# Performance work log

Measured on AMD Instinct MI355X. Metric: run time of the kernel, lower is better.

The kernel has to match this reference:

```python
import jax, jax.numpy as jnp
import numpy as np

B, C_IN, V, C_OUT, K = 4, 64, 50000, 128, 7


def setup_inputs() -> dict:
    key = jax.random.key(0)
    k1, k2, k3, k4 = jax.random.split(key, 4)
    x = jax.random.normal(k1, (B, C_IN, V, 1), dtype=jnp.float32)
    # Gi: per-vertex [self, n1, n2, n3] indices (random neighbors, in-range)
    Gi = jax.random.randint(k2, (B, V, 4), 0, V, dtype=jnp.int64)
    # Conv2d(in, out, kernel=(1,7)) weight collapsed to [out, in, 7]
    W = jax.random.normal(k3, (C_OUT, C_IN, K), dtype=jnp.float32) * 0.05
    b = jax.random.normal(k4, (C_OUT,), dtype=jnp.float32) * 0.05
    return {"x": x, "Gi": Gi, "W": W, "b": b}


def reference(x, Gi, W, b):
    xs = x[..., 0]  # [B, C, V]  (squeeze(-1))
    Bx, C, Vx = xs.shape
    # prepend zero-padding column (index 0 after Gi+1 maps padded -1 entries)
    xp = jnp.concatenate([jnp.zeros((Bx, C, 1), xs.dtype), xs], axis=2)  # [B,C,V+1]
    gi = Gi + 1
    # gather per batch: f[b,c,v,j] = xp[b,c,gi[b,v,j]]
    f = jax.vmap(lambda xb, gb: xb[:, gb])(xp, gi)  # [B, C, V, 4]
    f0, f1, f2, f3 = f[..., 0], f[..., 1], f[..., 2], f[..., 3]
    G = jnp.stack([
        f0,
        f1 + f2 + f3,                                        # symm_oper 1
        f1 * f2 * f3,                                        # symm_oper 2
        f1 * f2 + f1 * f3 + f2 * f3,                         # symm_oper 3
        f1 * f1 + f2 * f2 + f3 * f3,                         # symm_oper 4
        jnp.abs(f1 - f2) + jnp.abs(f1 - f3) + jnp.abs(f2 - f3),  # symm_oper 5
        f1 * f1 * f1 + f2 * f2 * f2 + f3 * f3 * f3,          # symm_oper 6
    ], axis=3)  # [B, C, V, 7]
    # conv2d with kernel (1,7), no padding -> width collapses to 1
    out = jnp.einsum('bcvk,ock->bov', G, W) + b[None, :, None]
    return out[..., None]  # [B, C_out, V, 1]
```

## Files before the change

kernel.cpp:

```cpp
#include <hip/hip_runtime.h>
#include <hip/hip_bf16.h>
#include <cstdint>
#include <cstddef>

#define BB   4
#define CIN  64
#define VV   50000
#define COUT 128
#define NV   32
#define KTOT 448
#define KT   14
#define PITCH 456

typedef __attribute__((ext_vector_type(8))) short short8;
typedef __attribute__((ext_vector_type(4))) float f32x4;

__device__ float          g_xt[(size_t)BB * VV * CIN];
__device__ unsigned short g_wb[KT * 8 * 64 * 8];

__device__ inline unsigned short f2bf(float f) {
    union { __hip_bfloat16 h; unsigned short u; } cv;
    cv.h = __float2bfloat16(f);
    return cv.u;
}

__global__ __launch_bounds__(256) void transpose_k(const float* __restrict__ x) {
    __shared__ float tile[64][65];
    int b  = blockIdx.y;
    int v0 = blockIdx.x * 64;
    int t  = threadIdx.x;
    int tv = t & 15;
    int tc = t >> 4;
#pragma unroll
    for (int i = 0; i < 4; i++) {
        int c = tc + 16 * i;
        int v = v0 + tv * 4;
        const float* src = x + ((size_t)b * CIN + c) * VV + v;
        float4 f;
        if (v + 3 < VV) {
            f = *(const float4*)src;
        } else {
            f.x = v + 0 < VV ? src[0] : 0.f;
            f.y = v + 1 < VV ? src[1] : 0.f;
            f.z = v + 2 < VV ? src[2] : 0.f;
            f.w = v + 3 < VV ? src[3] : 0.f;
        }
        tile[c][tv * 4 + 0] = f.x;
        tile[c][tv * 4 + 1] = f.y;
        tile[c][tv * 4 + 2] = f.z;
        tile[c][tv * 4 + 3] = f.w;
    }
    __syncthreads();
    int c4  = t & 15;
    int tvv = t >> 4;
#pragma unroll
    for (int i = 0; i < 4; i++) {
        int v = v0 + tvv + 16 * i;
        if (v < VV) {
            float4 f;
            f.x = tile[c4 * 4 + 0][tvv + 16 * i];
            f.y = tile[c4 * 4 + 1][tvv + 16 * i];
            f.z = tile[c4 * 4 + 2][tvv + 16 * i];
            f.w = tile[c4 * 4 + 3][tvv + 16 * i];
            *(float4*)(g_xt + ((size_t)b * VV + v) * CIN + c4 * 4) = f;
        }
    }
}

__global__ __launch_bounds__(256) void pack_wb_k(const float* __restrict__ W) {
    int idx = blockIdx.x * 256 + threadIdx.x;
    if (idx >= KT * 8 * 64) return;
    int lane = idx & 63;
    int mt   = (idx >> 6) & 7;
    int kt   = idx >> 9;
    int m    = mt * 16 + (lane & 15);
    int kb   = kt * 32 + (lane >> 4) * 8;
    union { unsigned short s[8]; short8 v; } u;
#pragma unroll
    for (int j = 0; j < 8; j++) {
        int kk = kb + j;
        int c  = kk & 63;
        int k  = kk >> 6;
        u.s[j] = f2bf(W[((size_t)m * CIN + c) * 7 + k]);
    }
    *(short8*)&g_wb[(size_t)idx * 8] = u.v;
}

__device__ inline void feats(float f0, float f1, float f2, float f3, float* g) {
    g[0] = f0;
    g[1] = f1 + f2 + f3;
    float p12 = f1 * f2, p13 = f1 * f3, p23 = f2 * f3;
    g[2] = p12 * f3;
    g[3] = p12 + p13 + p23;
    g[4] = f1 * f1 + f2 * f2 + f3 * f3;
    g[5] = fabsf(f1 - f2) + fabsf(f1 - f3) + fabsf(f2 - f3);
    g[6] = f1 * f1 * f1 + f2 * f2 * f2 + f3 * f3 * f3;
}

__global__ __launch_bounds__(256) void mesh_k(
        const void* __restrict__ Gi, const float* __restrict__ bias,
        float* __restrict__ out) {
    __shared__ unsigned short Gl[NV * PITCH];
    __shared__ int Sidx[NV][4];

    int b  = blockIdx.y;
    int v0 = blockIdx.x * NV;
    int t  = threadIdx.x;

    const unsigned* gu = (const unsigned*)Gi;
    bool is64 = ((gu[1] | gu[3] | gu[5] | gu[7]) == 0u);

    if (t < NV * 4) {
        int vv = t >> 2, j = t & 3;
        int v  = v0 + vv;
        long long val = 0;
        if (v < VV) {
            size_t gb = ((size_t)b * VV + v) * 4 + j;
            val = is64 ? ((const long long*)Gi)[gb] : (long long)((const int*)Gi)[gb];
        }
        Sidx[vv][j] = (int)(val < 0 ? 0 : (val >= VV ? VV - 1 : val));
    }
    __syncthreads();

    int lc2 = t & 31;
    int grp = t >> 5;
    int J[4][4];
#pragma unroll
    for (int p = 0; p < 4; ++p) {
        int vv = p * 8 + grp;
#pragma unroll
        for (int j = 0; j < 4; ++j) J[p][j] = Sidx[vv][j];
    }
    const float* base = g_xt + (size_t)b * VV * CIN + lc2 * 2;
    float2 F[4][4];
#pragma unroll
    for (int p = 0; p < 4; ++p)
#pragma unroll
        for (int j = 0; j < 4; ++j)
            F[p][j] = *(const float2*)(base + (size_t)J[p][j] * CIN);

#pragma unroll
    for (int p = 0; p < 4; ++p) {
        int vv = p * 8 + grp;
        unsigned* grow = (unsigned*)&Gl[vv * PITCH + lc2 * 2];
        float gx[7], gy[7];
        feats(F[p][0].x, F[p][1].x, F[p][2].x, F[p][3].x, gx);
        feats(F[p][0].y, F[p][1].y, F[p][2].y, F[p][3].y, gy);
#pragma unroll
        for (int k = 0; k < 7; k++)
            grow[k * 32] = (unsigned)f2bf(gx[k]) | ((unsigned)f2bf(gy[k]) << 16);
    }
    __syncthreads();

    int w    = t >> 6;
    int lane = t & 63;
    int l15  = lane & 15;
    int q    = lane >> 4;

    f32x4 acc[2][2] = {};

    const short8* wb = (const short8*)g_wb;
#pragma unroll 2
    for (int kt = 0; kt < KT; ++kt) {
        short8 a0 = wb[(kt * 8 + 2 * w    ) * 64 + lane];
        short8 a1 = wb[(kt * 8 + 2 * w + 1) * 64 + lane];
        short8 b0 = *(const short8*)&Gl[(l15     ) * PITCH + kt * 32 + q * 8];
        short8 b1 = *(const short8*)&Gl[(l15 + 16) * PITCH + kt * 32 + q * 8];
        acc[0][0] = __builtin_amdgcn_mfma_f32_16x16x32_bf16(a0, b0, acc[0][0], 0, 0, 0);
        acc[0][1] = __builtin_amdgcn_mfma_f32_16x16x32_bf16(a0, b1, acc[0][1], 0, 0, 0);
        acc[1][0] = __builtin_amdgcn_mfma_f32_16x16x32_bf16(a1, b0, acc[1][0], 0, 0, 0);
        acc[1][1] = __builtin_amdgcn_mfma_f32_16x16x32_bf16(a1, b1, acc[1][1], 0, 0, 0);
    }

#pragma unroll
    for (int mt = 0; mt < 2; ++mt) {
        int o = 32 * w + mt * 16 + q * 4;
        float bs[4];
#pragma unroll
        for (int r = 0; r < 4; ++r) bs[r] = bias[o + r];
#pragma unroll
        for (int nt = 0; nt < 2; ++nt) {
            int v = v0 + nt * 16 + l15;
            if (v < VV) {
                float* po = out + ((size_t)b * COUT + o) * VV + v;
#pragma unroll
                for (int r = 0; r < 4; ++r)
                    po[(size_t)r * VV] = acc[mt][nt][r] + bs[r];
            }
        }
    }
}

extern "C" void kernel_launch(void* const* d_in, const int* in_sizes, int n_in,
                              void* d_out, int out_size, void* d_ws, size_t ws_size,
                              hipStream_t stream) {
    const float* x    = (const float*)d_in[0];
    const void*  Gi   = d_in[1];
    const float* W    = (const float*)d_in[2];
    const float* bias = (const float*)d_in[3];
    float* out        = (float*)d_out;

    dim3 gt((VV + 63) / 64, BB);
    transpose_k<<<gt, 256, 0, stream>>>(x);
    pack_wb_k<<<(KT * 8 * 64 + 255) / 256, 256, 0, stream>>>(W);
    dim3 gm((VV + NV - 1) / NV, BB);
    mesh_k<<<gm, 256, 0, stream>>>(Gi, bias, out);
}
```

Baseline: 219.1 us.

## Store transposed activations in fp16 and switch MFMA from bf16 to fp16

The transposed activation buffer is now stored in fp16 instead of fp32, which halves the transpose write traffic and the random-gather read traffic in the mesh kernel. The gather is remapped so each thread loads half4 (4 channels) for 2 vertices instead of float2 for 4. Weights and features are packed as fp16 and the matrix multiply uses the f16 MFMA instead of bf16. The risk is fp16 range: cubic features of inputs near 3 or more lose precision, and larger values could overflow.

```diff
diff --git a/kernel.cpp b/kernel.cpp
--- a/kernel.cpp
+++ b/kernel.cpp
@@ -1,5 +1,4 @@
 #include <hip/hip_runtime.h>
-#include <hip/hip_bf16.h>
 #include <cstdint>
 #include <cstddef>
 
@@ -12,15 +11,17 @@
 #define KT   14
 #define PITCH 456
 
-typedef __attribute__((ext_vector_type(8))) short short8;
-typedef __attribute__((ext_vector_type(4))) float f32x4;
-
-__device__ float          g_xt[(size_t)BB * VV * CIN];
+typedef __attribute__((ext_vector_type(8))) short    short8;
+typedef __attribute__((ext_vector_type(8))) _Float16 half8;
+typedef __attribute__((ext_vector_type(4))) _Float16 half4;
+typedef __attribute__((ext_vector_type(4))) float    f32x4;
+
+__device__ _Float16       g_xt[(size_t)BB * VV * CIN];
 __device__ unsigned short g_wb[KT * 8 * 64 * 8];
 
-__device__ inline unsigned short f2bf(float f) {
-    union { __hip_bfloat16 h; unsigned short u; } cv;
-    cv.h = __float2bfloat16(f);
+__device__ inline unsigned short f2h(float f) {
+    union { _Float16 h; unsigned short u; } cv;
+    cv.h = (_Float16)f;
     return cv.u;
 }
 
@@ -51,18 +52,17 @@
         tile[c][tv * 4 + 3] = f.w;
     }
     __syncthreads();
-    int c4  = t & 15;
-    int tvv = t >> 4;
-#pragma unroll
-    for (int i = 0; i < 4; i++) {
-        int v = v0 + tvv + 16 * i;
+    int c8  = t & 7;
+    int tvv = t >> 3;
+#pragma unroll
+    for (int i = 0; i < 2; i++) {
+        int v = v0 + tvv + 32 * i;
         if (v < VV) {
-            float4 f;
-            f.x = tile[c4 * 4 + 0][tvv + 16 * i];
-            f.y = tile[c4 * 4 + 1][tvv + 16 * i];
-            f.z = tile[c4 * 4 + 2][tvv + 16 * i];
-            f.w = tile[c4 * 4 + 3][tvv + 16 * i];
-            *(float4*)(g_xt + ((size_t)b * VV + v) * CIN + c4 * 4) = f;
+            union { _Float16 h[8]; short8 s; } u;
+#pragma unroll
+            for (int j = 0; j < 8; j++)
+                u.h[j] = (_Float16)tile[c8 * 8 + j][tvv + 32 * i];
+            *(short8*)(g_xt + ((size_t)b * VV + v) * CIN + c8 * 8) = u.s;
         }
     }
 }
@@ -81,7 +81,7 @@
         int kk = kb + j;
         int c  = kk & 63;
         int k  = kk >> 6;
-        u.s[j] = f2bf(W[((size_t)m * CIN + c) * 7 + k]);
+        u.s[j] = f2h(W[((size_t)m * CIN + c) * 7 + k]);
     }
     *(short8*)&g_wb[(size_t)idx * 8] = u.v;
 }
@@ -100,7 +100,7 @@
 __global__ __launch_bounds__(256) void mesh_k(
         const void* __restrict__ Gi, const float* __restrict__ bias,
         float* __restrict__ out) {
-    __shared__ unsigned short Gl[NV * PITCH];
+    __shared__ _Float16 Gl[NV * PITCH];
     __shared__ int Sidx[NV][4];
 
     int b  = blockIdx.y;
@@ -122,33 +122,39 @@
     }
     __syncthreads();
 
-    int lc2 = t & 31;
-    int grp = t >> 5;
-    int J[4][4];
-#pragma unroll
-    for (int p = 0; p < 4; ++p) {
-        int vv = p * 8 + grp;
+    int c4   = t & 15;
+    int slot = t >> 4;
+    int J[2][4];
+#pragma unroll
+    for (int p = 0; p < 2; ++p) {
+        int vv = slot + p * 16;
 #pragma unroll
         for (int j = 0; j < 4; ++j) J[p][j] = Sidx[vv][j];
     }
-    const float* base = g_xt + (size_t)b * VV * CIN + lc2 * 2;
-    float2 F[4][4];
-#pragma unroll
-    for (int p = 0; p < 4; ++p)
+    const _Float16* base = g_xt + (size_t)b * VV * CIN + c4 * 4;
+    half4 F[2][4];
+#pragma unroll
+    for (int p = 0; p < 2; ++p)
 #pragma unroll
         for (int j = 0; j < 4; ++j)
-            F[p][j] = *(const float2*)(base + (size_t)J[p][j] * CIN);
-
-#pragma unroll
-    for (int p = 0; p < 4; ++p) {
-        int vv = p * 8 + grp;
-        unsigned* grow = (unsigned*)&Gl[vv * PITCH + lc2 * 2];
-        float gx[7], gy[7];
-        feats(F[p][0].x, F[p][1].x, F[p][2].x, F[p][3].x, gx);
-        feats(F[p][0].y, F[p][1].y, F[p][2].y, F[p][3].y, gy);
-#pragma unroll
-        for (int k = 0; k < 7; k++)
-            grow[k * 32] = (unsigned)f2bf(gx[k]) | ((unsigned)f2bf(gy[k]) << 16);
+            F[p][j] = *(const half4*)(base + (size_t)J[p][j] * CIN);
+
+#pragma unroll
+    for (int p = 0; p < 2; ++p) {
+        int vv = slot + p * 16;
+        float gc[4][7];
+#pragma unroll
+        for (int i = 0; i < 4; ++i)
+            feats((float)F[p][0][i], (float)F[p][1][i],
+                  (float)F[p][2][i], (float)F[p][3][i], gc[i]);
+        _Float16* grow = &Gl[vv * PITCH + c4 * 4];
+#pragma unroll
+        for (int k = 0; k < 7; k++) {
+            union { _Float16 h[4]; half4 v; } u;
+#pragma unroll
+            for (int i = 0; i < 4; ++i) u.h[i] = (_Float16)gc[i][k];
+            *(half4*)(grow + k * 64) = u.v;
+        }
     }
     __syncthreads();
 
@@ -159,17 +165,17 @@
 
     f32x4 acc[2][2] = {};
 
-    const short8* wb = (const short8*)g_wb;
+    const half8* wb = (const half8*)g_wb;
 #pragma unroll 2
     for (int kt = 0; kt < KT; ++kt) {
-        short8 a0 = wb[(kt * 8 + 2 * w    ) * 64 + lane];
-        short8 a1 = wb[(kt * 8 + 2 * w + 1) * 64 + lane];
-        short8 b0 = *(const short8*)&Gl[(l15     ) * PITCH + kt * 32 + q * 8];
-        short8 b1 = *(const short8*)&Gl[(l15 + 16) * PITCH + kt * 32 + q * 8];
-        acc[0][0] = __builtin_amdgcn_mfma_f32_16x16x32_bf16(a0, b0, acc[0][0], 0, 0, 0);
-        acc[0][1] = __builtin_amdgcn_mfma_f32_16x16x32_bf16(a0, b1, acc[0][1], 0, 0, 0);
-        acc[1][0] = __builtin_amdgcn_mfma_f32_16x16x32_bf16(a1, b0, acc[1][0], 0, 0, 0);
-        acc[1][1] = __builtin_amdgcn_mfma_f32_16x16x32_bf16(a1, b1, acc[1][1], 0, 0, 0);
+        half8 a0 = wb[(kt * 8 + 2 * w    ) * 64 + lane];
+        half8 a1 = wb[(kt * 8 + 2 * w + 1) * 64 + lane];
+        half8 b0 = *(const half8*)&Gl[(l15     ) * PITCH + kt * 32 + q * 8];
+        half8 b1 = *(const half8*)&Gl[(l15 + 16) * PITCH + kt * 32 + q * 8];
+        acc[0][0] = __builtin_amdgcn_mfma_f32_16x16x32_f16(a0, b0, acc[0][0], 0, 0, 0);
+        acc[0][1] = __builtin_amdgcn_mfma_f32_16x16x32_f16(a0, b1, acc[0][1], 0, 0, 0);
+        acc[1][0] = __builtin_amdgcn_mfma_f32_16x16x32_f16(a1, b0, acc[1][0], 0, 0, 0);
+        acc[1][1] = __builtin_amdgcn_mfma_f32_16x16x32_f16(a1, b1, acc[1][1], 0, 0, 0);
     }
 
 #pragma unroll
```

Result: faster. 205.0 us (-6.5%).
